# Kernel tuning notes

Hardware: AMD Instinct MI355X
Metric: run time of the kernel (lower is better)

The kernel has to match this reference:

```python
import jax, jax.numpy as jnp
import numpy as np

E = 8        # n_experts
TOP_K = 2    # n_activated_experts
B, T, C = 4, 2048, 2048   # batch, seq, d_model
F = 5632     # expert FFN hidden (SwiGLU)


def setup_inputs() -> dict:
    key = jax.random.key(0)
    k = jax.random.split(key, 5)
    s = 0.02  # init scale keeps activations sane
    return {
        "x":  jax.random.normal(k[0], (B, T, C), jnp.float32),
        "Wg": jax.random.normal(k[1], (C, E), jnp.float32) * s,   # gate Linear (no bias)
        "W1": jax.random.normal(k[2], (E, C, F), jnp.float32) * s, # expert gate proj
        "W3": jax.random.normal(k[3], (E, C, F), jnp.float32) * s, # expert up proj
        "W2": jax.random.normal(k[4], (E, F, C), jnp.float32) * s, # expert down proj
    }


def _moe(x, Wg, W1, W3, W2, top_k=TOP_K, norm_probs=True):
    Bb, Tt, Cc = x.shape
    xf = x.reshape(-1, Cc)                                   # [N, C]
    logits = xf @ Wg                                         # [N, E]
    probs = jax.nn.softmax(logits.astype(jnp.float32), axis=-1)
    probs, indices = jax.lax.top_k(probs, top_k)             # [N, K]
    if norm_probs:
        probs = probs / probs.sum(axis=-1, keepdims=True)
    probs = probs.astype(x.dtype)
    N, Ee = xf.shape[0], W1.shape[0]
    # per-token combine weights: w[n, e] = prob if expert e selected for token n else 0
    # (top_k indices are distinct per token, so at most one add per (n, e))
    w = jnp.zeros((N, Ee), x.dtype).at[jnp.arange(N)[:, None], indices].add(probs)
    # scan over experts: weight-0 tokens contribute nothing, matching the sparse
    # masked dispatch/scatter-add of the original exactly.
    def body(y, ws):
        w1, w3, w2, we = ws                                   # we: [N]
        h = jax.nn.silu(xf @ w1) * (xf @ w3)                  # [N, F]
        return y + we[:, None] * (h @ w2), None
    y, _ = jax.lax.scan(body, jnp.zeros_like(xf), (W1, W3, W2, w.T))
    return y.reshape(Bb, Tt, Cc)


def reference(x, Wg, W1, W3, W2):
    return _moe(x, Wg, W1, W3, W2)
```

## Files before the change

kernel.cpp:

```cpp
#include <hip/hip_runtime.h>

#define N_TOK 8192
#define C_DIM 2048
#define F_DIM 5632
#define E_NUM 8
#define BK 64

#define BM 256
#define MAXT 72
#define BN1 128
#define NN1 (F_DIM/BN1)
#define GRID1 (MAXT * NN1)
#define BN2 256
#define KSPLIT 2
#define NN2 (C_DIM/BN2)
#define GRID2 (MAXT * NN2 * KSPLIT)
#define NT1 (C_DIM/BK)
#define NT2H (F_DIM/BK/KSPLIT)
#define KHALF (F_DIM/KSPLIT)

#define PRE_R 2048
#define PRE_T 67584
#define GRID_PRE (PRE_R + PRE_T)

typedef __attribute__((ext_vector_type(8))) short bf16x8;
typedef __attribute__((ext_vector_type(4))) float f32x4;

typedef const void __attribute__((address_space(1)))* gas1;
typedef void __attribute__((address_space(3)))* las3;

__device__ __forceinline__ unsigned short f2bf(float f){
  union { float f; unsigned u; } v; v.f = f;
  unsigned r = v.u + 0x7FFFu + ((v.u >> 16) & 1u);
  return (unsigned short)(r >> 16);
}

__device__ __forceinline__ void glds16(const unsigned short* g, unsigned short* l){
  __builtin_amdgcn_global_load_lds((gas1)g, (las3)l, 16, 0, 0);
}

#define MFMA_BF16 __builtin_amdgcn_mfma_f32_16x16x32_bf16

#define BAR1_VM(N) do{ asm volatile("s_waitcnt vmcnt(" #N ")" ::: "memory"); \
    __builtin_amdgcn_sched_barrier(0); __builtin_amdgcn_s_barrier(); \
    __builtin_amdgcn_sched_barrier(0); } while(0)
#define BAR2() do{ asm volatile("s_waitcnt lgkmcnt(0)" ::: "memory"); \
    __builtin_amdgcn_sched_barrier(0); __builtin_amdgcn_s_barrier(); \
    __builtin_amdgcn_sched_barrier(0); } while(0)

__global__ __launch_bounds__(256) void k_pre(
    const float* __restrict__ x, const float* __restrict__ Wg,
    const float* __restrict__ W1, const float* __restrict__ W3,
    const float* __restrict__ W2,
    int* __restrict__ cnt, int* __restrict__ list, float* __restrict__ p_slot,
    unsigned short* __restrict__ xb, unsigned short* __restrict__ wb13,
    unsigned short* __restrict__ wb2)
{
  __shared__ float t[64][65];
  int bid = blockIdx.x;
  int tid = threadIdx.x;

  if (bid < PRE_R){
    int wid = tid >> 6, lane = tid & 63;
    int n = bid * 4 + wid;
    int e = lane >> 3, sub = lane & 7;
    const float* xr = x + (size_t)n * C_DIM;
    float acc = 0.f;
    for (int i0 = sub*4; i0 < C_DIM; i0 += 32){
      float4 v = *(const float4*)&xr[i0];
      acc += v.x * Wg[(i0  )*E_NUM + e];
      acc += v.y * Wg[(i0+1)*E_NUM + e];
      acc += v.z * Wg[(i0+2)*E_NUM + e];
      acc += v.w * Wg[(i0+3)*E_NUM + e];
    }
    acc += __shfl_xor(acc, 1);
    acc += __shfl_xor(acc, 2);
    acc += __shfl_xor(acc, 4);
    float lg[E_NUM];
    #pragma unroll
    for (int j = 0; j < E_NUM; ++j) lg[j] = __shfl(acc, j*8);
    unsigned short* xbr = xb + (size_t)n * C_DIM;
    #pragma unroll
    for (int i0 = lane*4; i0 < C_DIM; i0 += 256){
      float4 v = *(const float4*)&xr[i0];
      ushort4 u; u.x = f2bf(v.x); u.y = f2bf(v.y); u.z = f2bf(v.z); u.w = f2bf(v.w);
      *(ushort4*)&xbr[i0] = u;
    }
    if (lane == 0){
      int e1 = 0; float m1 = lg[0];
      #pragma unroll
      for (int j = 1; j < E_NUM; ++j) if (lg[j] > m1){ m1 = lg[j]; e1 = j; }
      int e2 = -1; float m2 = -1e30f;
      #pragma unroll
      for (int j = 0; j < E_NUM; ++j) if (j != e1 && lg[j] > m2){ m2 = lg[j]; e2 = j; }
      float p1 = 1.f / (1.f + __expf(m2 - m1));
      float p2 = 1.f - p1;
      int pos1 = atomicAdd(&cnt[e1], 1);
      list[e1*N_TOK + pos1] = n*2;
      p_slot[n*2] = p1;
      int pos2 = atomicAdd(&cnt[e2], 1);
      list[e2*N_TOK + pos2] = n*2 + 1;
      p_slot[n*2 + 1] = p2;
    }
    return;
  }
  int rel = bid - PRE_R;
  int z = rel / 2816;
  int r2 = rel - z*2816;
  int tx = tid & 63, ty = tid >> 6;
  if (z < 16){
    int fx = r2 % 88, cy = r2 / 88;
    const float* in = ((z < 8) ? W1 : W3) + (size_t)(z & 7) * C_DIM * F_DIM;
    unsigned short* out = wb13 + (size_t)z * C_DIM * F_DIM;
    int c0 = fx*64, r0 = cy*64;
    #pragma unroll
    for (int i = 0; i < 16; ++i){
      int r = ty + i*4;
      t[r][tx] = in[(size_t)(r0 + r) * F_DIM + c0 + tx];
    }
    __syncthreads();
    #pragma unroll
    for (int i = 0; i < 16; ++i){
      int cr = ty + i*4;
      out[(size_t)(c0 + cr) * C_DIM + r0 + tx] = f2bf(t[tx][cr]);
    }
  } else {
    int cx = r2 % 32, fy = r2 / 32;
    const float* in = W2 + (size_t)(z - 16) * F_DIM * C_DIM;
    unsigned short* out = wb2 + (size_t)(z - 16) * C_DIM * F_DIM;
    int c0 = cx*64, r0 = fy*64;
    #pragma unroll
    for (int i = 0; i < 16; ++i){
      int r = ty + i*4;
      t[r][tx] = in[(size_t)(r0 + r) * C_DIM + c0 + tx];
    }
    __syncthreads();
    #pragma unroll
    for (int i = 0; i < 16; ++i){
      int cr = ty + i*4;
      out[(size_t)(c0 + cr) * F_DIM + r0 + tx] = f2bf(t[tx][cr]);
    }
  }
}

__global__ void k_prefix(const int* __restrict__ cnt, int* __restrict__ meta){
  if (threadIdx.x == 0 && blockIdx.x == 0){
    int acc = 0, t = 0;
    for (int e = 0; e < E_NUM; ++e){
      meta[e] = acc; acc += cnt[e];
      int nt = (cnt[e] + BM - 1) / BM;
      for (int i = 0; i < nt; ++i) meta[16 + t++] = (e << 16) | i;
    }
    meta[8] = t;
  }
}

__global__ __launch_bounds__(512, 2) void k_gemm1(
    const unsigned short* __restrict__ xb,
    const unsigned short* __restrict__ wb1,
    const unsigned short* __restrict__ wb3,
    unsigned short* __restrict__ h,
    const int* __restrict__ cnt,
    const int* __restrict__ meta,
    const int* __restrict__ list)
{
  __shared__ __align__(16) unsigned short lds[2*32768];
  int o = blockIdx.x;
  int tid = threadIdx.x;

  int xcd = o & 7, idx = o >> 3;
  int t = (idx / NN1) * 8 + xcd;
  int n0 = (idx % NN1) * BN1;
  if (t >= meta[8]) return;
  int info = meta[16 + t];
  int e  = info >> 16;
  int m0 = (info & 0xffff) * BM;
  int count = cnt[e];
  int hbase = meta[e];

  int lane = tid & 63, wid = tid >> 6;
  int wm = wid >> 1, wn = wid & 1;
  int l15 = lane & 15;
  int xc0 = (lane >> 4) ^ (lane & 7);
  int xc1 = xc0 ^ 4;

  int srow = tid >> 3;
  int swz = ((tid & 7) ^ (srow & 7)) * 8;
  const unsigned short* aP[4];
  #pragma unroll
  for (int u = 0; u < 4; ++u){
    int ts = list[e*N_TOK + m0 + u*64 + srow];
    int tok = (ts >> 1) & (N_TOK - 1);
    aP[u] = xb + (size_t)tok * C_DIM + swz;
  }
  const unsigned short* bP[4];
  #pragma unroll
  for (int u = 0; u < 4; ++u){
    const unsigned short* base = (u < 2) ? wb1 : wb3;
    bP[u] = base + ((size_t)e*F_DIM + n0 + (u & 1)*64 + srow) * C_DIM + swz;
  }
  int ldw = wid * 512;

  #define ST_A(u, kt) glds16(aP[u] + (kt)*BK, &lds[((kt)&1)*32768 + (u)*4096 + ldw])
  #define ST_B(u, kt) glds16(bP[u] + (kt)*BK, &lds[((kt)&1)*32768 + 16384 + (u)*4096 + ldw])
  #define READ_A(d, buf) do{ _Pragma("unroll") for (int m_ = 0; m_ < 4; ++m_){ \
      int row_ = wm*64 + m_*16 + l15; \
      d[m_][0] = *(const bf16x8*)&(buf)[row_*64 + xc0*8]; \
      d[m_][1] = *(const bf16x8*)&(buf)[row_*64 + xc1*8]; } }while(0)
  #define READ_B(d1, d3, buf, q) do{ int brow_ = wn*64 + (q)*16 + l15; \
      d1[0] = *(const bf16x8*)&(buf)[16384 + brow_*64 + xc0*8]; \
      d1[1] = *(const bf16x8*)&(buf)[16384 + brow_*64 + xc1*8]; \
      d3[0] = *(const bf16x8*)&(buf)[24576 + brow_*64 + xc0*8]; \
      d3[1] = *(const bf16x8*)&(buf)[24576 + brow_*64 + xc1*8]; }while(0)
  #define MFMA16(q, b1, b3) do{ _Pragma("unroll") for (int m_ = 0; m_ < 4; ++m_){ \
      acc1[m_][q] = MFMA_BF16(a[m_][0], b1[0], acc1[m_][q], 0, 0, 0); \
      acc1[m_][q] = MFMA_BF16(a[m_][1], b1[1], acc1[m_][q], 0, 0, 0); \
      acc3[m_][q] = MFMA_BF16(a[m_][0], b3[0], acc3[m_][q], 0, 0, 0); \
      acc3[m_][q] = MFMA_BF16(a[m_][1], b3[1], acc3[m_][q], 0, 0, 0); } }while(0)

  ST_A(0,0); ST_A(1,0); ST_A(2,0); ST_A(3,0);
  ST_B(0,0); ST_B(1,0); ST_B(2,0); ST_B(3,0);
  ST_A(0,1); ST_A(1,1); ST_A(2,1); ST_A(3,1);
  asm volatile("s_waitcnt vmcnt(4)" ::: "memory");
  __builtin_amdgcn_sched_barrier(0);
  __builtin_amdgcn_s_barrier();
  __builtin_amdgcn_sched_barrier(0);

  f32x4 zero = {0.f, 0.f, 0.f, 0.f};
  f32x4 acc1[4][4], acc3[4][4];
  #pragma unroll
  for (int m = 0; m < 4; ++m)
    #pragma unroll
    for (int q = 0; q < 4; ++q){ acc1[m][q] = zero; acc3[m][q] = zero; }

  bf16x8 a[4][2];
  READ_A(a, lds);
  bf16x8 bX1[2], bX3[2], bY1[2], bY3[2];
  READ_B(bX1, bX3, lds, 0);

  for (int kt = 0; kt < NT1; ++kt){
    const unsigned short* bufc = &lds[(kt & 1)*32768];
    const unsigned short* bufn = &lds[((kt+1) & 1)*32768];
    ST_B(0, kt+1); ST_B(1, kt+1); ST_B(2, kt+1); ST_B(3, kt+1);
    READ_B(bY1, bY3, bufc, 1);
    __builtin_amdgcn_s_setprio(1);
    MFMA16(0, bX1, bX3);
    __builtin_amdgcn_s_setprio(0);
    ST_A(0, kt+2); ST_A(1, kt+2);
    READ_B(bX1, bX3, bufc, 2);
    __builtin_amdgcn_s_setprio(1);
    MFMA16(1, bY1, bY3);
    __builtin_amdgcn_s_setprio(0);
    ST_A(2, kt+2); ST_A(3, kt+2);
    READ_B(bY1, bY3, bufc, 3);
    __builtin_amdgcn_s_setprio(1);
    MFMA16(2, bX1, bX3);
    __builtin_amdgcn_s_setprio(0);
    BAR1_VM(4);
    bf16x8 an[4][2];
    READ_A(an, bufn);
    READ_B(bX1, bX3, bufn, 0);
    __builtin_amdgcn_s_setprio(1);
    MFMA16(3, bY1, bY3);
    __builtin_amdgcn_s_setprio(0);
    BAR2();
    #pragma unroll
    for (int m = 0; m < 4; ++m){ a[m][0] = an[m][0]; a[m][1] = an[m][1]; }
  }
  asm volatile("s_waitcnt vmcnt(0)" ::: "memory");

  #pragma unroll
  for (int m = 0; m < 4; ++m){
    #pragma unroll
    for (int r = 0; r < 4; ++r){
      int rloc = m0 + wm*64 + m*16 + ((lane >> 4) * 4) + r;
      if (rloc < count){
        unsigned short* hrow = h + (size_t)(hbase + rloc) * F_DIM + n0 + wn*64 + l15;
        #pragma unroll
        for (int q = 0; q < 4; ++q){
          float v1 = acc1[m][q][r];
          float v3 = acc3[m][q][r];
          float hv = (v1 / (1.f + __expf(-v1))) * v3;
          hrow[q*16] = f2bf(hv);
        }
      }
    }
  }
  #undef ST_A
  #undef ST_B
  #undef READ_A
  #undef READ_B
  #undef MFMA16
}

__global__ __launch_bounds__(512, 2) void k_gemm2(
    const unsigned short* __restrict__ h,
    const unsigned short* __restrict__ wb2,
    unsigned short* __restrict__ ybuf,
    const int* __restrict__ cnt,
    const int* __restrict__ meta,
    const int* __restrict__ list)
{
  int o = blockIdx.x;
  int tid = threadIdx.x;
  int xcd = o & 7, idx = o >> 3;
  int ks = idx / 72;
  int r2 = idx % 72;
  int t = (r2 / NN2) * 8 + xcd;
  int n0 = (r2 % NN2) * BN2;
  if (t >= meta[8]) return;
  int info = meta[16 + t];
  int e  = info >> 16;
  int m0 = (info & 0xffff) * BM;
  int count = cnt[e];
  int hbase = meta[e];

  __shared__ __align__(16) unsigned short lds[2*32768];

  int lane = tid & 63, wid = tid >> 6;
  int wm = wid >> 1, wn = wid & 1;
  int l15 = lane & 15;
  int xc0 = (lane >> 4) ^ (lane & 7);
  int xc1 = xc0 ^ 4;

  int srow = tid >> 3;
  int swz = ((tid & 7) ^ (srow & 7)) * 8;
  size_t kb0 = (size_t)ks * KHALF;
  const unsigned short* aP[4];
  #pragma unroll
  for (int u = 0; u < 4; ++u)
    aP[u] = h + (size_t)(hbase + m0 + u*64 + srow) * F_DIM + kb0 + swz;
  const unsigned short* bP[4];
  #pragma unroll
  for (int u = 0; u < 4; ++u)
    bP[u] = wb2 + ((size_t)e*C_DIM + n0 + u*64 + srow) * F_DIM + kb0 + swz;
  int ldw = wid * 512;

  #define ST_A2(u, kt) glds16(aP[u] + (kt)*BK, &lds[((kt)&1)*32768 + (u)*4096 + ldw])
  #define ST_B2(u, kt) glds16(bP[u] + (kt)*BK, &lds[((kt)&1)*32768 + 16384 + (u)*4096 + ldw])
  #define READ_A2(d, buf) do{ _Pragma("unroll") for (int m_ = 0; m_ < 4; ++m_){ \
      int row_ = wm*64 + m_*16 + l15; \
      d[m_][0] = *(const bf16x8*)&(buf)[row_*64 + xc0*8]; \
      d[m_][1] = *(const bf16x8*)&(buf)[row_*64 + xc1*8]; } }while(0)
  #define READ_B2(d, buf, q) do{ _Pragma("unroll") for (int j_ = 0; j_ < 2; ++j_){ \
      int brow_ = wn*128 + ((q)*2 + j_)*16 + l15; \
      d[j_][0] = *(const bf16x8*)&(buf)[16384 + brow_*64 + xc0*8]; \
      d[j_][1] = *(const bf16x8*)&(buf)[16384 + brow_*64 + xc1*8]; } }while(0)
  #define MFMA2(qb, d) do{ _Pragma("unroll") for (int m_ = 0; m_ < 4; ++m_) \
      _Pragma("unroll") for (int j_ = 0; j_ < 2; ++j_){ \
        acc[m_][(qb)*2+j_] = MFMA_BF16(a[m_][0], d[j_][0], acc[m_][(qb)*2+j_], 0, 0, 0); \
        acc[m_][(qb)*2+j_] = MFMA_BF16(a[m_][1], d[j_][1], acc[m_][(qb)*2+j_], 0, 0, 0); } }while(0)

  ST_A2(0,0); ST_A2(1,0); ST_A2(2,0); ST_A2(3,0);
  ST_B2(0,0); ST_B2(1,0); ST_B2(2,0); ST_B2(3,0);
  asm volatile("s_waitcnt vmcnt(4)" ::: "memory");
  ST_A2(0,1); ST_A2(1,1); ST_A2(2,1); ST_A2(3,1);
  ST_B2(0,1); ST_B2(2,1);
  asm volatile("s_waitcnt vmcnt(6)" ::: "memory");
  __builtin_amdgcn_sched_barrier(0);
  __builtin_amdgcn_s_barrier();
  __builtin_amdgcn_sched_barrier(0);

  f32x4 zero = {0.f, 0.f, 0.f, 0.f};
  f32x4 acc[4][8];
  #pragma unroll
  for (int m = 0; m < 4; ++m)
    #pragma unroll
    for (int nf = 0; nf < 8; ++nf) acc[m][nf] = zero;

  bf16x8 a[4][2];
  READ_A2(a, lds);
  bf16x8 bfX[2][2], bfY[2][2];
  READ_B2(bfX, lds, 0);

  for (int kt = 0; kt < NT2H; ++kt){
    const unsigned short* bufc = &lds[(kt & 1)*32768];
    const unsigned short* bufn = &lds[((kt+1) & 1)*32768];
    ST_B2(1, kt+1); ST_B2(3, kt+1);
    READ_B2(bfY, bufc, 1);
    __builtin_amdgcn_s_setprio(1);
    MFMA2(0, bfX);
    __builtin_amdgcn_s_setprio(0);
    ST_A2(0, kt+2); ST_A2(1, kt+2);
    READ_B2(bfX, bufc, 2);
    __builtin_amdgcn_s_setprio(1);
    MFMA2(1, bfY);
    __builtin_amdgcn_s_setprio(0);
    ST_A2(2, kt+2); ST_A2(3, kt+2);
    READ_B2(bfY, bufc, 3);
    __builtin_amdgcn_s_setprio(1);
    MFMA2(2, bfX);
    __builtin_amdgcn_s_setprio(0);
    ST_B2(0, kt+2); ST_B2(2, kt+2);
    BAR1_VM(6);
    bf16x8 an[4][2];
    READ_A2(an, bufn);
    READ_B2(bfX, bufn, 0);
    __builtin_amdgcn_s_setprio(1);
    MFMA2(3, bfY);
    __builtin_amdgcn_s_setprio(0);
    BAR2();
    #pragma unroll
    for (int m = 0; m < 4; ++m){ a[m][0] = an[m][0]; a[m][1] = an[m][1]; }
  }
  asm volatile("s_waitcnt vmcnt(0)" ::: "memory");

  #pragma unroll
  for (int m = 0; m < 4; ++m){
    #pragma unroll
    for (int r = 0; r < 4; ++r){
      int rloc = m0 + wm*64 + m*16 + ((lane >> 4) * 4) + r;
      if (rloc < count){
        int ts = list[e*N_TOK + rloc];
        unsigned short* yr = ybuf + ((size_t)ks*(2*N_TOK) + ts)*C_DIM + n0 + wn*128 + l15;
        #pragma unroll
        for (int nf = 0; nf < 8; ++nf)
          yr[nf*16] = f2bf(acc[m][nf][r]);
      }
    }
  }
  #undef ST_A2
  #undef ST_B2
  #undef READ_A2
  #undef READ_B2
  #undef MFMA2
}

__global__ __launch_bounds__(256) void k_combine(
    const unsigned short* __restrict__ ybuf,
    const float* __restrict__ p_slot,
    float* __restrict__ y)
{
  const int CW = C_DIM/8;
  int i = blockIdx.x * blockDim.x + threadIdx.x;
  int stride = gridDim.x * blockDim.x;
  const size_t KS_OFF = (size_t)(2*N_TOK) * C_DIM;
  for (; i < N_TOK*CW; i += stride){
    int n = i >> 8;
    int c0 = (i & 255) * 8;
    size_t b1 = (size_t)(2*n)   * C_DIM + c0;
    size_t b2 = (size_t)(2*n+1) * C_DIM + c0;
    ushort4 a0 = *(const ushort4*)&ybuf[b1];
    ushort4 a1 = *(const ushort4*)&ybuf[b1+4];
    ushort4 a2 = *(const ushort4*)&ybuf[KS_OFF + b1];
    ushort4 a3 = *(const ushort4*)&ybuf[KS_OFF + b1+4];
    ushort4 c2 = *(const ushort4*)&ybuf[b2];
    ushort4 c3 = *(const ushort4*)&ybuf[b2+4];
    ushort4 d2 = *(const ushort4*)&ybuf[KS_OFF + b2];
    ushort4 d3 = *(const ushort4*)&ybuf[KS_OFF + b2+4];
    float p1 = p_slot[2*n], p2 = p_slot[2*n+1];
    float out[8];
    #define B2F(u) __builtin_bit_cast(float, (unsigned)(u) << 16)
    out[0] = p1*(B2F(a0.x)+B2F(a2.x)) + p2*(B2F(c2.x)+B2F(d2.x));
    out[1] = p1*(B2F(a0.y)+B2F(a2.y)) + p2*(B2F(c2.y)+B2F(d2.y));
    out[2] = p1*(B2F(a0.z)+B2F(a2.z)) + p2*(B2F(c2.z)+B2F(d2.z));
    out[3] = p1*(B2F(a0.w)+B2F(a2.w)) + p2*(B2F(c2.w)+B2F(d2.w));
    out[4] = p1*(B2F(a1.x)+B2F(a3.x)) + p2*(B2F(c3.x)+B2F(d3.x));
    out[5] = p1*(B2F(a1.y)+B2F(a3.y)) + p2*(B2F(c3.y)+B2F(d3.y));
    out[6] = p1*(B2F(a1.z)+B2F(a3.z)) + p2*(B2F(c3.z)+B2F(d3.z));
    out[7] = p1*(B2F(a1.w)+B2F(a3.w)) + p2*(B2F(c3.w)+B2F(d3.w));
    #undef B2F
    float4* yo = (float4*)&y[(size_t)n * C_DIM + c0];
    yo[0] = *(float4*)&out[0];
    yo[1] = *(float4*)&out[4];
  }
}

extern "C" void kernel_launch(void* const* d_in, const int* in_sizes, int n_in,
                              void* d_out, int out_size, void* d_ws, size_t ws_size,
                              hipStream_t stream)
{
  const float* x  = (const float*)d_in[0];
  const float* Wg = (const float*)d_in[1];
  const float* W1 = (const float*)d_in[2];
  const float* W3 = (const float*)d_in[3];
  const float* W2 = (const float*)d_in[4];
  float* y = (float*)d_out;
  (void)in_sizes; (void)n_in; (void)out_size; (void)ws_size;

  char* ws = (char*)d_ws;
  size_t o = 0;
  auto alloc = [&](size_t bytes)->char* {
    char* p = ws + o;
    o = (o + bytes + 255) & ~(size_t)255;
    return p;
  };
  int*    cnt    = (int*)  alloc(E_NUM * 4);
  int*    meta   = (int*)  alloc(160 * 4);
  float*  p_slot = (float*)alloc((size_t)2*N_TOK * 4);
  int*    list   = (int*)  alloc((size_t)E_NUM*N_TOK * 4);
  unsigned short* xb  = (unsigned short*)alloc((size_t)N_TOK*C_DIM * 2 + 65536);
  unsigned short* wb1 = (unsigned short*)alloc((size_t)E_NUM*C_DIM*F_DIM * 2);
  unsigned short* wb3 = (unsigned short*)alloc((size_t)E_NUM*C_DIM*F_DIM * 2);
  unsigned short* wb2 = (unsigned short*)alloc((size_t)E_NUM*C_DIM*F_DIM * 2);
  unsigned short* h   = (unsigned short*)alloc((size_t)(2*N_TOK + 1024)*F_DIM * 2 + 65536);
  unsigned short* ybuf= (unsigned short*)alloc((size_t)KSPLIT*2*N_TOK*C_DIM * 2);
  (void)wb3;

  hipMemsetAsync(cnt, 0, E_NUM * 4, stream);
  k_pre<<<GRID_PRE, 256, 0, stream>>>(x, Wg, W1, W3, W2, cnt, list, p_slot, xb, wb1, wb2);
  k_prefix<<<1, 64, 0, stream>>>(cnt, meta);
  k_gemm1<<<GRID1, 512, 0, stream>>>(xb, wb1, wb3, h, cnt, meta, list);
  k_gemm2<<<GRID2, 512, 0, stream>>>(h, wb2, ybuf, cnt, meta, list);
  k_combine<<<4096, 256, 0, stream>>>(ybuf, p_slot, y);
}
```

Baseline: 1.731 ms.

## Raise GEMM2 split-K to four and remap block order across XCDs

Doubles the split-K factor of the down-projection GEMM so each block covers a quarter of F, giving more blocks to spread across CUs. Both GEMM kernels change how block IDs map to tiles: each XCD now takes a contiguous chunk of work, with the tile index varying fastest so blocks running together share weight columns. The combine kernel is generalized to sum KSPLIT partials, and the partial-output buffer now reuses the bf16 W1 workspace region, which is no longer needed after GEMM1. The trade-off is twice as much bf16 partial-output traffic to write and read back in the combine step.

```diff
diff --git a/kernel.cpp b/kernel.cpp
--- a/kernel.cpp
+++ b/kernel.cpp
@@ -12,7 +12,7 @@
 #define NN1 (F_DIM/BN1)
 #define GRID1 (MAXT * NN1)
 #define BN2 256
-#define KSPLIT 2
+#define KSPLIT 4
 #define NN2 (C_DIM/BN2)
 #define GRID2 (MAXT * NN2 * KSPLIT)
 #define NT1 (C_DIM/BK)
@@ -168,9 +168,9 @@
   int o = blockIdx.x;
   int tid = threadIdx.x;
 
-  int xcd = o & 7, idx = o >> 3;
-  int t = (idx / NN1) * 8 + xcd;
-  int n0 = (idx % NN1) * BN1;
+  int w = (o & 7) * (GRID1/8) + (o >> 3);
+  int t = w % MAXT;
+  int n0 = (w / MAXT) * BN1;
   if (t >= meta[8]) return;
   int info = meta[16 + t];
   int e  = info >> 16;
@@ -303,11 +303,11 @@
 {
   int o = blockIdx.x;
   int tid = threadIdx.x;
-  int xcd = o & 7, idx = o >> 3;
-  int ks = idx / 72;
-  int r2 = idx % 72;
-  int t = (r2 / NN2) * 8 + xcd;
-  int n0 = (r2 % NN2) * BN2;
+  int w = (o & 7) * (GRID2/8) + (o >> 3);
+  int ks = w / (GRID2/KSPLIT);
+  int r2 = w % (GRID2/KSPLIT);
+  int t = r2 % MAXT;
+  int n0 = (r2 / MAXT) * BN2;
   if (t >= meta[8]) return;
   int info = meta[16 + t];
   int e  = info >> 16;
@@ -440,26 +440,26 @@
     int c0 = (i & 255) * 8;
     size_t b1 = (size_t)(2*n)   * C_DIM + c0;
     size_t b2 = (size_t)(2*n+1) * C_DIM + c0;
-    ushort4 a0 = *(const ushort4*)&ybuf[b1];
-    ushort4 a1 = *(const ushort4*)&ybuf[b1+4];
-    ushort4 a2 = *(const ushort4*)&ybuf[KS_OFF + b1];
-    ushort4 a3 = *(const ushort4*)&ybuf[KS_OFF + b1+4];
-    ushort4 c2 = *(const ushort4*)&ybuf[b2];
-    ushort4 c3 = *(const ushort4*)&ybuf[b2+4];
-    ushort4 d2 = *(const ushort4*)&ybuf[KS_OFF + b2];
-    ushort4 d3 = *(const ushort4*)&ybuf[KS_OFF + b2+4];
+    float s1[8] = {0,0,0,0,0,0,0,0};
+    float s2[8] = {0,0,0,0,0,0,0,0};
+    #define B2F(u) __builtin_bit_cast(float, (unsigned)(u) << 16)
+    #pragma unroll
+    for (int ks = 0; ks < KSPLIT; ++ks){
+      size_t off = (size_t)ks * KS_OFF;
+      ushort4 a0 = *(const ushort4*)&ybuf[off + b1];
+      ushort4 a1 = *(const ushort4*)&ybuf[off + b1 + 4];
+      ushort4 c0v = *(const ushort4*)&ybuf[off + b2];
+      ushort4 c1v = *(const ushort4*)&ybuf[off + b2 + 4];
+      s1[0] += B2F(a0.x); s1[1] += B2F(a0.y); s1[2] += B2F(a0.z); s1[3] += B2F(a0.w);
+      s1[4] += B2F(a1.x); s1[5] += B2F(a1.y); s1[6] += B2F(a1.z); s1[7] += B2F(a1.w);
+      s2[0] += B2F(c0v.x); s2[1] += B2F(c0v.y); s2[2] += B2F(c0v.z); s2[3] += B2F(c0v.w);
+      s2[4] += B2F(c1v.x); s2[5] += B2F(c1v.y); s2[6] += B2F(c1v.z); s2[7] += B2F(c1v.w);
+    }
+    #undef B2F
     float p1 = p_slot[2*n], p2 = p_slot[2*n+1];
     float out[8];
-    #define B2F(u) __builtin_bit_cast(float, (unsigned)(u) << 16)
-    out[0] = p1*(B2F(a0.x)+B2F(a2.x)) + p2*(B2F(c2.x)+B2F(d2.x));
-    out[1] = p1*(B2F(a0.y)+B2F(a2.y)) + p2*(B2F(c2.y)+B2F(d2.y));
-    out[2] = p1*(B2F(a0.z)+B2F(a2.z)) + p2*(B2F(c2.z)+B2F(d2.z));
-    out[3] = p1*(B2F(a0.w)+B2F(a2.w)) + p2*(B2F(c2.w)+B2F(d2.w));
-    out[4] = p1*(B2F(a1.x)+B2F(a3.x)) + p2*(B2F(c3.x)+B2F(d3.x));
-    out[5] = p1*(B2F(a1.y)+B2F(a3.y)) + p2*(B2F(c3.y)+B2F(d3.y));
-    out[6] = p1*(B2F(a1.z)+B2F(a3.z)) + p2*(B2F(c3.z)+B2F(d3.z));
-    out[7] = p1*(B2F(a1.w)+B2F(a3.w)) + p2*(B2F(c3.w)+B2F(d3.w));
-    #undef B2F
+    #pragma unroll
+    for (int j = 0; j < 8; ++j) out[j] = p1*s1[j] + p2*s2[j];
     float4* yo = (float4*)&y[(size_t)n * C_DIM + c0];
     yo[0] = *(float4*)&out[0];
     yo[1] = *(float4*)&out[4];
@@ -494,7 +494,7 @@
   unsigned short* wb3 = (unsigned short*)alloc((size_t)E_NUM*C_DIM*F_DIM * 2);
   unsigned short* wb2 = (unsigned short*)alloc((size_t)E_NUM*C_DIM*F_DIM * 2);
   unsigned short* h   = (unsigned short*)alloc((size_t)(2*N_TOK + 1024)*F_DIM * 2 + 65536);
-  unsigned short* ybuf= (unsigned short*)alloc((size_t)KSPLIT*2*N_TOK*C_DIM * 2);
+  unsigned short* ybuf = wb1;
   (void)wb3;
 
   hipMemsetAsync(cnt, 0, E_NUM * 4, stream);
```

Result: no change. 1.745 ms (+0.8%).
